# Kernel optimization log

Hardware: AMD Instinct MI355X
Metric: run time of the kernel (lower is better)

The kernel has to match this reference:

```python
import jax, jax.numpy as jnp
import numpy as np
from jax import lax
from jax.scipy.special import logsumexp

B, T, K = 256, 1024, 64


def setup_inputs() -> dict:
    key = jax.random.key(0)
    k1, k2, k3 = jax.random.split(key, 3)
    y_true = jax.random.randint(k1, (B, T), 0, K)  # 0 == pad tag
    emissions = jax.random.normal(k2, (B, T, K), dtype=jnp.float32)
    transition = jax.random.normal(k3, (K, K), dtype=jnp.float32) * 0.1
    return {"y_true": y_true, "emissions": emissions, "transition": transition}


def _log_partition(emissions, mask, transition):
    # alpha_0 = emissions[:, 0, :] (TF code does not mask step 0)
    alpha0 = emissions[:, 0, :]  # [B, K]

    def step(alpha, xs):
        emit_t, m_t = xs  # [B, K], [B]
        # score[b, i, j] = alpha[b, i] + transition[i, j] + emit_t[b, j]
        score = alpha[:, :, None] + transition[None, :, :] + emit_t[:, None, :]
        new_a = logsumexp(score, axis=1)  # [B, K]
        new_a = jnp.where(m_t[:, None] > 0, new_a, alpha)
        return new_a, None

    xs = (jnp.swapaxes(emissions[:, 1:, :], 0, 1),  # [T-1, B, K]
          jnp.swapaxes(mask[:, 1:], 0, 1))           # [T-1, B]
    alpha, _ = lax.scan(step, alpha0, xs)
    return logsumexp(alpha, axis=1)  # [B]


def reference(y_true, emissions, transition):
    mask = (y_true != 0).astype(emissions.dtype)  # [B, T]
    yt = y_true.astype(jnp.int32)

    # emission scores of the gold path on masked emissions
    em_masked = emissions * mask[:, :, None]
    e_scores = jnp.take_along_axis(em_masked, yt[:, :, None], axis=2)[..., 0].sum(axis=1)  # [B]

    # transition scores of the gold path
    prev, nxt = yt[:, :-1], yt[:, 1:]
    t_scores = (transition[prev, nxt] * mask[:, 1:]).sum(axis=1)  # [B]

    log_z = _log_partition(emissions, mask, transition)  # [B]
    ll = e_scores + t_scores - log_z
    return -jnp.mean(ll)
```

## Files before the change

kernel.cpp:

```cpp
#include <hip/hip_runtime.h>

#define LOG2E 1.44269504088896340736f
#define LN2   0.69314718055994530942f

typedef short bf8 __attribute__((ext_vector_type(8)));
typedef float f4  __attribute__((ext_vector_type(4)));

static __device__ __forceinline__ unsigned short f2bf_rne(float f) {
    unsigned u = __float_as_uint(f);
    u += 0x7FFFu + ((u >> 16) & 1u);
    return (unsigned short)(u >> 16);
}
static __device__ __forceinline__ unsigned pack_bf_trunc(float lo, float hi) {
    return __builtin_amdgcn_perm(__float_as_uint(hi), __float_as_uint(lo), 0x07060302u);
}

__global__ __attribute__((amdgpu_flat_work_group_size(256, 256), amdgpu_waves_per_eu(4)))
void crf_scan(const int* __restrict__ yg, const float* __restrict__ em,
              const float* __restrict__ tr, unsigned short* __restrict__ Pg)
{
    constexpr int T = 1024;
    const int c = blockIdx.x, b = blockIdx.y;
    const int tid = threadIdx.x;
    const int w = tid >> 6;
    const int lane = tid & 63, nl = lane & 15, q = lane >> 4;

    __shared__ __align__(16) float d_sh[4][64];

    bf8 afr[4][2];
    #pragma unroll
    for (int mt = 0; mt < 4; ++mt) {
        const int g = 32 * (mt >> 1) + 8 * (nl >> 2) + 4 * (mt & 1) + (nl & 3);
        #pragma unroll
        for (int ka = 0; ka < 2; ++ka) {
            bf8 v;
            #pragma unroll
            for (int j = 0; j < 8; ++j) {
                const int k = 32 * ka + 8 * q + j;
                v[j] = (short)f2bf_rne(exp2f(tr[k * 64 + g] * LOG2E));
            }
            afr[mt][ka] = v;
        }
    }

    bf8 bfr[2];
    #pragma unroll
    for (int kt = 0; kt < 2; ++kt) {
        bf8 v;
        #pragma unroll
        for (int j = 0; j < 8; ++j)
            v[j] = (short)((32 * kt + 8 * q + j == 16 * w + nl) ? 0x3F80 : 0);
        bfr[kt] = v;
    }

    const int t0 = 1 + 64 * c;
    const int nsteps = (c == 15) ? 63 : 64;
    const float* emb = em + (size_t)b * T * 64;

    int tl = t0 + lane; if (tl > T - 1) tl = T - 1;
    const int yvl = yg[b * T + tl];
    const unsigned long long msk = __ballot(lane < nsteps && yvl != 0);

    float ldc = emb[t0 * 64 + lane];
    for (int s = 0; s < nsteps; ++s) {
        int tn = t0 + s + 1; if (tn > T - 1) tn = T - 1;
        const float ldn = emb[tn * 64 + lane];
        if ((msk >> s) & 1ull) {
            d_sh[w][lane] = exp2f(ldc * LOG2E - 7.0f);
            f4 dq[4];
            #pragma unroll
            for (int mt = 0; mt < 4; ++mt)
                dq[mt] = *(const f4*)&d_sh[w][32 * (mt >> 1) + 4 * (mt & 1) + 8 * q];
            f4 acc[4];
            #pragma unroll
            for (int mt = 0; mt < 4; ++mt) {
                f4 a = __builtin_amdgcn_mfma_f32_16x16x32_bf16(
                           afr[mt][0], bfr[0], (f4)(0.0f), 0, 0, 0);
                acc[mt] = __builtin_amdgcn_mfma_f32_16x16x32_bf16(
                           afr[mt][1], bfr[1], a, 0, 0, 0);
            }
            #pragma unroll
            for (int kt = 0; kt < 2; ++kt) {
                union { uint4 u; bf8 v8; } wv;
                wv.u.x = pack_bf_trunc(acc[2*kt  ][0] * dq[2*kt  ][0],
                                       acc[2*kt  ][1] * dq[2*kt  ][1]);
                wv.u.y = pack_bf_trunc(acc[2*kt  ][2] * dq[2*kt  ][2],
                                       acc[2*kt  ][3] * dq[2*kt  ][3]);
                wv.u.z = pack_bf_trunc(acc[2*kt+1][0] * dq[2*kt+1][0],
                                       acc[2*kt+1][1] * dq[2*kt+1][1]);
                wv.u.w = pack_bf_trunc(acc[2*kt+1][2] * dq[2*kt+1][2],
                                       acc[2*kt+1][3] * dq[2*kt+1][3]);
                bfr[kt] = wv.v8;
            }
        }
        ldc = ldn;
    }

    unsigned short* pg = Pg + ((size_t)(b * 16 + c) << 12);
    #pragma unroll
    for (int kt = 0; kt < 2; ++kt)
        *(uint4*)(pg + (16 * w + nl) * 64 + 32 * kt + 8 * q) =
            *(const uint4*)&bfr[kt];
}

__global__ __attribute__((amdgpu_flat_work_group_size(256, 256)))
void crf_combine(const int* __restrict__ yg, const float* __restrict__ em,
                 const float* __restrict__ tr, const unsigned short* __restrict__ Pg,
                 float* __restrict__ out)
{
    constexpr int T = 1024;
    const int b = blockIdx.x, tid = threadIdx.x;
    const int w = tid >> 6, j = tid & 63;

    __shared__ __align__(16) float v_sh[64];
    __shared__ float red[3][4];

    float ep = 0.f, tp = 0.f; int cnt = 0;
    float v = 0.f, L = 0.f, vs = 0.f;

    if (w == 0) {
        const float e0 = em[(size_t)b * T * 64 + j];
        float M0 = e0;
        #pragma unroll
        for (int o = 32; o > 0; o >>= 1) M0 = fmaxf(M0, __shfl_xor(M0, o, 64));
        v = exp2f((e0 - M0) * LOG2E);
        L = M0;

        const unsigned short* row = Pg + ((size_t)(b * 16) << 12) + j * 64;
        uint4 pA[8], pB[8];
        #pragma unroll
        for (int r = 0; r < 8; ++r) pA[r] = *(const uint4*)(row + r * 8);

#define CHUNK_STEP(CUR, NXT, CIDX)                                                 \
        do {                                                                       \
            if ((CIDX) + 1 < 16) {      \
                const unsigned short* rn = row + ((size_t)((CIDX) + 1) << 12);     \
                _Pragma("unroll")                                                  \
                for (int r = 0; r < 8; ++r) NXT[r] = *(const uint4*)(rn + r * 8);  \
            }                                                                      \
            v_sh[j] = v;                             \
            float s0 = 0.f, s1 = 0.f, s2 = 0.f, s3 = 0.f;                          \
            _Pragma("unroll")                                                      \
            for (int r = 0; r < 8; ++r) {                                          \
                const uint4 qq = CUR[r];                                           \
                const float* vp = &v_sh[r * 8];                                    \
                s0 = fmaf(__uint_as_float(qq.x << 16),         vp[0], s0);         \
                s1 = fmaf(__uint_as_float(qq.x & 0xFFFF0000u), vp[1], s1);         \
                s2 = fmaf(__uint_as_float(qq.y << 16),         vp[2], s2);         \
                s3 = fmaf(__uint_as_float(qq.y & 0xFFFF0000u), vp[3], s3);         \
                s0 = fmaf(__uint_as_float(qq.z << 16),         vp[4], s0);         \
                s1 = fmaf(__uint_as_float(qq.z & 0xFFFF0000u), vp[5], s1);         \
                s2 = fmaf(__uint_as_float(qq.w << 16),         vp[6], s2);         \
                s3 = fmaf(__uint_as_float(qq.w & 0xFFFF0000u), vp[7], s3);         \
            }                                                                      \
            float s = (s0 + s1) + (s2 + s3);                                       \
            const unsigned sb =                                                    \
                (unsigned)__builtin_amdgcn_readlane((int)__float_as_uint(s), 0);   \
            const int ef = (int)((sb >> 23) & 0xFF);                               \
            if (ef > 0 && ef < 255 && ef != 127) {       \
                const int E = ef - 127;                                            \
                s *= __uint_as_float((unsigned)(127 - E) << 23);                   \
                L += (float)E * LN2;                                               \
            }                                                                      \
            v = s;                                                                 \
        } while (0)

        for (int cc = 0; cc < 16; cc += 2) {
            CHUNK_STEP(pA, pB, cc);
            CHUNK_STEP(pB, pA, cc + 1);
        }
#undef CHUNK_STEP

        vs = v;
        #pragma unroll
        for (int o = 32; o > 0; o >>= 1) vs += __shfl_xor(vs, o, 64);
    } else {
        const int* yb = yg + b * T;
        const int wt = tid - 64;
        for (int t = 1 + wt; t < T; t += 192) {
            const int yt = yb[t];
            if (yt != 0) {
                ++cnt;
                tp += tr[yb[t - 1] * 64 + yt];
                ep += em[((size_t)b * T + t) * 64 + yt];
            }
        }
        if (tid == 64) {
            const int y0 = yb[0];
            if (y0 != 0) ep += em[(size_t)b * T * 64 + y0];
        }
        #pragma unroll
        for (int o = 32; o > 0; o >>= 1) {
            ep  += __shfl_xor(ep, o, 64);
            tp  += __shfl_xor(tp, o, 64);
            cnt += __shfl_xor(cnt, o, 64);
        }
        if (j == 0) { red[0][w] = ep; red[1][w] = tp; red[2][w] = (float)cnt; }
    }
    __syncthreads();

    if (tid == 0) {
        const float eps = red[0][1] + red[0][2] + red[0][3];
        const float tps = red[1][1] + red[1][2] + red[1][3];
        const float cs  = red[2][1] + red[2][2] + red[2][3];
        const float logz = L + 7.0f * LN2 * cs + __log2f(vs) * LN2;
        atomicAdd(out, (eps + tps - logz) * (-1.0f / 256.0f));
    }
}

extern "C" void kernel_launch(void* const* d_in, const int* in_sizes, int n_in,
                              void* d_out, int out_size, void* d_ws, size_t ws_size,
                              hipStream_t stream) {
    const int*   y  = (const int*)d_in[0];
    const float* em = (const float*)d_in[1];
    const float* tr = (const float*)d_in[2];
    float* out = (float*)d_out;
    unsigned short* Pg = (unsigned short*)d_ws;

    hipMemsetAsync(out, 0, sizeof(float), stream);
    crf_scan<<<dim3(16, 256), dim3(256), 0, stream>>>(y, em, tr, Pg);
    crf_combine<<<dim3(256), dim3(256), 0, stream>>>(y, em, tr, Pg, out);
}
```

Baseline: 245.1 us.

## Halve scan block size, each wave computing two 16-column tiles with packed scaling

The scan kernel now runs 128 threads per block instead of 256, and each wave handles two 16-column slices of the chunk's transfer matrix. Both slices share the A fragments and the per-step scaling loads. Scaling multiplies use two-wide float vectors, which could map to packed FP32 ops. This cuts redundant per-wave work (emission exp and LDS stores) and the number of waves per step chain. The cost is a longer serial MFMA chain per wave and more registers, which may reduce latency hiding.

```diff
diff --git a/kernel.cpp b/kernel.cpp
--- a/kernel.cpp
+++ b/kernel.cpp
@@ -5,6 +5,7 @@
 
 typedef short bf8 __attribute__((ext_vector_type(8)));
 typedef float f4  __attribute__((ext_vector_type(4)));
+typedef float f2  __attribute__((ext_vector_type(2)));
 
 static __device__ __forceinline__ unsigned short f2bf_rne(float f) {
     unsigned u = __float_as_uint(f);
@@ -15,7 +16,7 @@
     return __builtin_amdgcn_perm(__float_as_uint(hi), __float_as_uint(lo), 0x07060302u);
 }
 
-__global__ __attribute__((amdgpu_flat_work_group_size(256, 256), amdgpu_waves_per_eu(4)))
+__global__ __attribute__((amdgpu_flat_work_group_size(128, 128), amdgpu_waves_per_eu(2, 4)))
 void crf_scan(const int* __restrict__ yg, const float* __restrict__ em,
               const float* __restrict__ tr, unsigned short* __restrict__ Pg)
 {
@@ -25,7 +26,7 @@
     const int w = tid >> 6;
     const int lane = tid & 63, nl = lane & 15, q = lane >> 4;
 
-    __shared__ __align__(16) float d_sh[4][64];
+    __shared__ __align__(16) float d_sh[2][64];
 
     bf8 afr[4][2];
     #pragma unroll
@@ -43,15 +44,17 @@
         }
     }
 
-    bf8 bfr[2];
+    bf8 bfr[2][2];
     #pragma unroll
-    for (int kt = 0; kt < 2; ++kt) {
-        bf8 v;
-        #pragma unroll
-        for (int j = 0; j < 8; ++j)
-            v[j] = (short)((32 * kt + 8 * q + j == 16 * w + nl) ? 0x3F80 : 0);
-        bfr[kt] = v;
-    }
+    for (int kt = 0; kt < 2; ++kt)
+        #pragma unroll
+        for (int u = 0; u < 2; ++u) {
+            bf8 v;
+            #pragma unroll
+            for (int j = 0; j < 8; ++j)
+                v[j] = (short)((32 * kt + 8 * q + j == 16 * (2 * w + u) + nl) ? 0x3F80 : 0);
+            bfr[kt][u] = v;
+        }
 
     const int t0 = 1 + 64 * c;
     const int nsteps = (c == 15) ? 63 : 64;
@@ -67,30 +70,39 @@
         const float ldn = emb[tn * 64 + lane];
         if ((msk >> s) & 1ull) {
             d_sh[w][lane] = exp2f(ldc * LOG2E - 7.0f);
-            f4 dq[4];
-            #pragma unroll
-            for (int mt = 0; mt < 4; ++mt)
-                dq[mt] = *(const f4*)&d_sh[w][32 * (mt >> 1) + 4 * (mt & 1) + 8 * q];
-            f4 acc[4];
+            f2 dp[4][2];
             #pragma unroll
             for (int mt = 0; mt < 4; ++mt) {
-                f4 a = __builtin_amdgcn_mfma_f32_16x16x32_bf16(
-                           afr[mt][0], bfr[0], (f4)(0.0f), 0, 0, 0);
-                acc[mt] = __builtin_amdgcn_mfma_f32_16x16x32_bf16(
-                           afr[mt][1], bfr[1], a, 0, 0, 0);
-            }
-            #pragma unroll
-            for (int kt = 0; kt < 2; ++kt) {
-                union { uint4 u; bf8 v8; } wv;
-                wv.u.x = pack_bf_trunc(acc[2*kt  ][0] * dq[2*kt  ][0],
-                                       acc[2*kt  ][1] * dq[2*kt  ][1]);
-                wv.u.y = pack_bf_trunc(acc[2*kt  ][2] * dq[2*kt  ][2],
-                                       acc[2*kt  ][3] * dq[2*kt  ][3]);
-                wv.u.z = pack_bf_trunc(acc[2*kt+1][0] * dq[2*kt+1][0],
-                                       acc[2*kt+1][1] * dq[2*kt+1][1]);
-                wv.u.w = pack_bf_trunc(acc[2*kt+1][2] * dq[2*kt+1][2],
-                                       acc[2*kt+1][3] * dq[2*kt+1][3]);
-                bfr[kt] = wv.v8;
+                const float* dsrc = &d_sh[w][32 * (mt >> 1) + 4 * (mt & 1) + 8 * q];
+                dp[mt][0] = *(const f2*)&dsrc[0];
+                dp[mt][1] = *(const f2*)&dsrc[2];
+            }
+            #pragma unroll
+            for (int u = 0; u < 2; ++u) {
+                f4 acc[4];
+                #pragma unroll
+                for (int mt = 0; mt < 4; ++mt) {
+                    f4 a = __builtin_amdgcn_mfma_f32_16x16x32_bf16(
+                               afr[mt][0], bfr[0][u], (f4)(0.0f), 0, 0, 0);
+                    acc[mt] = __builtin_amdgcn_mfma_f32_16x16x32_bf16(
+                               afr[mt][1], bfr[1][u], a, 0, 0, 0);
+                }
+                #pragma unroll
+                for (int kt = 0; kt < 2; ++kt) {
+                    f2 a0, a1, b0, b1;
+                    a0[0] = acc[2*kt  ][0]; a0[1] = acc[2*kt  ][1];
+                    a1[0] = acc[2*kt  ][2]; a1[1] = acc[2*kt  ][3];
+                    b0[0] = acc[2*kt+1][0]; b0[1] = acc[2*kt+1][1];
+                    b1[0] = acc[2*kt+1][2]; b1[1] = acc[2*kt+1][3];
+                    a0 *= dp[2*kt  ][0];  a1 *= dp[2*kt  ][1];
+                    b0 *= dp[2*kt+1][0];  b1 *= dp[2*kt+1][1];
+                    union { uint4 uu; bf8 v8; } wv;
+                    wv.uu.x = pack_bf_trunc(a0[0], a0[1]);
+                    wv.uu.y = pack_bf_trunc(a1[0], a1[1]);
+                    wv.uu.z = pack_bf_trunc(b0[0], b0[1]);
+                    wv.uu.w = pack_bf_trunc(b1[0], b1[1]);
+                    bfr[kt][u] = wv.v8;
+                }
             }
         }
         ldc = ldn;
@@ -98,9 +110,11 @@
 
     unsigned short* pg = Pg + ((size_t)(b * 16 + c) << 12);
     #pragma unroll
-    for (int kt = 0; kt < 2; ++kt)
-        *(uint4*)(pg + (16 * w + nl) * 64 + 32 * kt + 8 * q) =
-            *(const uint4*)&bfr[kt];
+    for (int u = 0; u < 2; ++u)
+        #pragma unroll
+        for (int kt = 0; kt < 2; ++kt)
+            *(uint4*)(pg + (16 * (2 * w + u) + nl) * 64 + 32 * kt + 8 * q) =
+                *(const uint4*)&bfr[kt][u];
 }
 
 __global__ __attribute__((amdgpu_flat_work_group_size(256, 256)))
@@ -218,6 +232,6 @@
     unsigned short* Pg = (unsigned short*)d_ws;
 
     hipMemsetAsync(out, 0, sizeof(float), stream);
-    crf_scan<<<dim3(16, 256), dim3(256), 0, stream>>>(y, em, tr, Pg);
+    crf_scan<<<dim3(16, 256), dim3(128), 0, stream>>>(y, em, tr, Pg);
     crf_combine<<<dim3(256), dim3(256), 0, stream>>>(y, em, tr, Pg, out);
 }
```

New measurement: 225.7 us. -7.9%, faster.
